# Optimization experiments

Hardware: AMD Instinct MI355X
Metric: run time of the kernel (lower is better)

The kernel has to match this reference:

```python
import jax, jax.numpy as jnp
import numpy as np

N_P, N_A, N_T = 20000, 10000, 5000
D_IN, D_OUT = 512, 256
E_P, E_A, E_T = 320000, 160000, 80000


def setup_inputs() -> dict:
    key = jax.random.key(0)
    ks = iter(jax.random.split(key, 64))

    def nrm(shape, scale=1.0):
        return jax.random.normal(next(ks), shape, dtype=jnp.float32) * scale

    def xav(shape):
        # xavier_uniform-like scale (gain 1.414), normal draw is fine for a baseline
        return nrm(shape, 1.414 * (2.0 / (shape[0] + shape[1])) ** 0.5)

    def edges(ne, n_src, n_dst):
        src = jax.random.randint(next(ks), (ne,), 0, n_src, dtype=jnp.int32)
        dst = jax.random.randint(next(ks), (ne,), 0, n_dst, dtype=jnp.int32)
        w = jax.random.uniform(next(ks), (ne,), dtype=jnp.float32) / 16.0  # ~normalized adj values
        return src, dst, w

    d = {}
    d["x_p"] = nrm((N_P, D_IN))
    d["x_a"] = nrm((N_A, D_IN))
    d["x_t"] = nrm((N_T, D_IN))
    d["e_p_a_src"], d["e_p_a_dst"], d["e_p_a_w"] = edges(E_P, N_A, N_P)
    d["e_p_t_src"], d["e_p_t_dst"], d["e_p_t_w"] = edges(E_P, N_T, N_P)
    d["e_a_p_src"], d["e_a_p_dst"], d["e_a_p_w"] = edges(E_A, N_P, N_A)
    d["e_a_t_src"], d["e_a_t_dst"], d["e_a_t_w"] = edges(E_A, N_T, N_A)
    d["e_t_p_src"], d["e_t_p_dst"], d["e_t_p_w"] = edges(E_T, N_P, N_T)
    d["e_t_a_src"], d["e_t_a_dst"], d["e_t_a_w"] = edges(E_T, N_A, N_T)
    # parameters for each target type k: W_proj per neighbor, w_self, w_share, w_att, w_cat, bias
    for k, nbs in (("p", ("a", "t")), ("a", ("p", "t")), ("t", ("p", "a"))):
        for nb in nbs:
            d[f"W_{k}_{nb}"] = xav((D_IN, D_OUT))
        d[f"ws_{k}"] = xav((D_IN, D_OUT))
        d[f"wsh_{k}"] = xav((D_OUT, D_OUT))
        d[f"watt_{k}"] = xav((2 * D_OUT, 1))
        d[f"wcat_{k}"] = xav((2 * D_OUT, D_OUT))
        d[f"b_{k}"] = xav((1, D_OUT))
    return d


def _hete_agg(x_self, w_self, w_share, w_att, w_cat, bias, nb_inputs):
    """nb_inputs: list of (x_nb, W_proj, src, dst, edge_w). Faithful to HeteAggregateLayer."""
    n = x_self.shape[0]
    self_ft = (x_self @ w_self) @ w_share  # [n, d]
    # per-relation: project -> spmm (gather + weighted segment-sum over dst) -> share
    nb_fts = [
        jax.ops.segment_sum((x_nb @ Wp)[src] * ew[:, None], dst, num_segments=n) @ w_share
        for (x_nb, Wp, src, dst, ew) in nb_inputs
    ]
    L = len(nb_fts)
    # e = leaky_relu(cat([cat(nb_ft,0), self_ft.repeat(L,1)],1) @ w_att)  -> [L*n, 1]
    e = jnp.concatenate(
        [jax.nn.leaky_relu(jnp.concatenate([f, self_ft], axis=1) @ w_att) for f in nb_fts],
        axis=0,
    )
    # NOTE: faithful replication of the original `e.view(-1, L)` reshape semantics
    att = jax.nn.softmax(e.reshape(n, L), axis=1)  # [n, L]
    agg = nb_fts[0] * att[:, 0:1]
    for i in range(1, L):
        agg = agg + nb_fts[i] * att[:, i : i + 1]
    return jnp.concatenate([agg, self_ft], axis=1) @ w_cat + bias


def reference(x_p, x_a, x_t,
              e_p_a_src, e_p_a_dst, e_p_a_w, e_p_t_src, e_p_t_dst, e_p_t_w,
              e_a_p_src, e_a_p_dst, e_a_p_w, e_a_t_src, e_a_t_dst, e_a_t_w,
              e_t_p_src, e_t_p_dst, e_t_p_w, e_t_a_src, e_t_a_dst, e_t_a_w,
              W_p_a, W_p_t, ws_p, wsh_p, watt_p, wcat_p, b_p,
              W_a_p, W_a_t, ws_a, wsh_a, watt_a, wcat_a, b_a,
              W_t_p, W_t_a, ws_t, wsh_t, watt_t, wcat_t, b_t):
    out_p = _hete_agg(x_p, ws_p, wsh_p, watt_p, wcat_p, b_p,
                      [(x_a, W_p_a, e_p_a_src, e_p_a_dst, e_p_a_w),
                       (x_t, W_p_t, e_p_t_src, e_p_t_dst, e_p_t_w)])
    out_a = _hete_agg(x_a, ws_a, wsh_a, watt_a, wcat_a, b_a,
                      [(x_p, W_a_p, e_a_p_src, e_a_p_dst, e_a_p_w),
                       (x_t, W_a_t, e_a_t_src, e_a_t_dst, e_a_t_w)])
    out_t = _hete_agg(x_t, ws_t, wsh_t, watt_t, wcat_t, b_t,
                      [(x_p, W_t_p, e_t_p_src, e_t_p_dst, e_t_p_w),
                       (x_a, W_t_a, e_t_a_src, e_t_a_dst, e_t_a_w)])
    return (out_p, out_a, out_t)
```

## Files before the change

kernel.cpp:

```cpp
#include <hip/hip_runtime.h>

namespace {

typedef short s16x8 __attribute__((ext_vector_type(8)));
typedef float f32x4 __attribute__((ext_vector_type(4)));

__device__ __forceinline__ float bf2f(unsigned short u) {
  return __uint_as_float(((unsigned)u) << 16);
}
__device__ __forceinline__ unsigned short f2bf(float f) {
  unsigned u = __float_as_uint(f);
  u += 0x7fffu + ((u >> 16) & 1u);
  return (unsigned short)(u >> 16);
}

typedef __attribute__((address_space(3))) unsigned int lds_u32;
typedef __attribute__((address_space(1))) const unsigned int glob_u32;
__device__ __forceinline__ void gl16(const void* g, void* l) {
  __builtin_amdgcn_global_load_lds((glob_u32*)g, (lds_u32*)l, 16, 0, 0);
}

__global__ __launch_bounds__(256) void cvt_x3(const float* __restrict__ x0,
                                              const float* __restrict__ x1,
                                              const float* __restrict__ x2,
                                              unsigned short* __restrict__ out) {
  size_t i = ((size_t)blockIdx.x * 256 + threadIdx.x) * 8;
  const float* src;
  size_t off;
  if (i < (size_t)20000 * 512) { src = x0; off = i; }
  else if (i < (size_t)30000 * 512) { src = x1; off = i - (size_t)20000 * 512; }
  else { src = x2; off = i - (size_t)30000 * 512; }
  float4 a = *(const float4*)(src + off);
  float4 b = *(const float4*)(src + off + 4);
  s16x8 v;
  v[0] = (short)f2bf(a.x); v[1] = (short)f2bf(a.y);
  v[2] = (short)f2bf(a.z); v[3] = (short)f2bf(a.w);
  v[4] = (short)f2bf(b.x); v[5] = (short)f2bf(b.y);
  v[6] = (short)f2bf(b.z); v[7] = (short)f2bf(b.w);
  *(s16x8*)(out + i) = v;
}

struct Tc6 { const float* src[6]; unsigned short* dst[6]; int R[6]; };
__global__ __launch_bounds__(256) void transpose_cvt(Tc6 a) {
  int mat = blockIdx.z;
  int R = a.R[mat];
  int r0 = blockIdx.y * 32, c0 = blockIdx.x * 32;
  if (r0 >= R) return;
  const float* __restrict__ src = a.src[mat];
  unsigned short* __restrict__ dst = a.dst[mat];
  __shared__ float T[32][33];
  int tx = threadIdx.x & 31, ty = threadIdx.x >> 5;
  #pragma unroll
  for (int j = 0; j < 4; ++j) {
    int r = ty + j * 8;
    T[r][tx] = src[(size_t)(r0 + r) * 256 + c0 + tx];
  }
  __syncthreads();
  #pragma unroll
  for (int j = 0; j < 4; ++j) {
    int c = ty + j * 8;
    dst[(size_t)(c0 + c) * R + r0 + tx] = f2bf(T[tx][c]);
  }
}

struct Comb9 { const unsigned short* A[9]; const float* B[9]; unsigned short* C[9]; };
__global__ __launch_bounds__(256) void combine_mfma(Comb9 g) {
  int z = blockIdx.z;
  const unsigned short* __restrict__ A = g.A[z];
  const float* __restrict__ B = g.B[z];
  unsigned short* __restrict__ C = g.C[z];
  int row0 = blockIdx.y * 128;
  int col0 = blockIdx.x * 128;
  __shared__ unsigned short As[128 * 40];
  __shared__ unsigned short Bs[128 * 40];
  int tid = threadIdx.x, lane = tid & 63, w = tid >> 6;
  int quad = lane >> 4, m16 = lane & 15;
  f32x4 acc[2][8];
  #pragma unroll
  for (int r = 0; r < 2; ++r)
    #pragma unroll
    for (int c = 0; c < 8; ++c) acc[r][c] = (f32x4){0.f, 0.f, 0.f, 0.f};
  for (int k0 = 0; k0 < 256; k0 += 32) {
    #pragma unroll
    for (int i = 0; i < 2; ++i) {
      int ch = tid + i * 256;
      int m = ch >> 2, kk = (ch & 3) * 8;
      *(s16x8*)&As[m * 40 + kk] = *(const s16x8*)(A + (size_t)(row0 + m) * 256 + k0 + kk);
      const float4* bp = (const float4*)(B + (size_t)(col0 + m) * 256 + k0 + kk);
      float4 b0 = bp[0], b1 = bp[1];
      s16x8 bv;
      bv[0] = (short)f2bf(b0.x); bv[1] = (short)f2bf(b0.y);
      bv[2] = (short)f2bf(b0.z); bv[3] = (short)f2bf(b0.w);
      bv[4] = (short)f2bf(b1.x); bv[5] = (short)f2bf(b1.y);
      bv[6] = (short)f2bf(b1.z); bv[7] = (short)f2bf(b1.w);
      *(s16x8*)&Bs[m * 40 + kk] = bv;
    }
    __syncthreads();
    s16x8 af[2], bf[8];
    #pragma unroll
    for (int r = 0; r < 2; ++r)
      af[r] = *(const s16x8*)&As[(w * 32 + r * 16 + m16) * 40 + quad * 8];
    #pragma unroll
    for (int c = 0; c < 8; ++c)
      bf[c] = *(const s16x8*)&Bs[(c * 16 + m16) * 40 + quad * 8];
    #pragma unroll
    for (int r = 0; r < 2; ++r)
      #pragma unroll
      for (int c = 0; c < 8; ++c)
        acc[r][c] = __builtin_amdgcn_mfma_f32_16x16x32_bf16(af[r], bf[c], acc[r][c], 0, 0, 0);
    __syncthreads();
  }
  #pragma unroll
  for (int r = 0; r < 2; ++r)
    #pragma unroll
    for (int i = 0; i < 4; ++i) {
      int row = row0 + w * 32 + r * 16 + quad * 4 + i;
      #pragma unroll
      for (int c = 0; c < 8; ++c)
        C[(size_t)row * 512 + col0 + c * 16 + m16] = f2bf(acc[r][c][i]);
    }
}

struct Proj9 { const unsigned short* A[9]; const unsigned short* Bt[9]; unsigned short* C[9]; int M[9]; };
__global__ __launch_bounds__(256) void proj_mfma9(Proj9 g) {
  int z = blockIdx.z;
  int M = g.M[z];
  int row0 = blockIdx.y * 128;
  if (row0 >= M) return;
  int col0 = blockIdx.x * 128;
  const unsigned short* __restrict__ A = g.A[z];
  const unsigned short* __restrict__ Bt = g.Bt[z];
  unsigned short* __restrict__ C = g.C[z];
  __shared__ unsigned short As[128 * 32];
  __shared__ unsigned short Bs[128 * 32];
  int tid = threadIdx.x, lane = tid & 63, w = tid >> 6;
  int quad = lane >> 4, m16 = lane & 15;
  int lr = lane >> 2, lk = (lane & 3) * 8;
  int r0g = row0 + w * 32 + lr;
  int r1g = r0g + 16;
  const unsigned short* a0p = A + (size_t)(r0g < M ? r0g : M - 1) * 512 + lk;
  const unsigned short* a1p = A + (size_t)(r1g < M ? r1g : M - 1) * 512 + lk;
  const unsigned short* b0p = Bt + (size_t)(col0 + w * 32 + lr) * 512 + lk;
  const unsigned short* b1p = b0p + (size_t)16 * 512;
  unsigned short* as0 = &As[w * 1024];
  unsigned short* as1 = &As[w * 1024 + 512];
  unsigned short* bs0 = &Bs[w * 1024];
  unsigned short* bs1 = &Bs[w * 1024 + 512];
  int wr = (w & 1) * 64, wc = (w >> 1) * 64;
  f32x4 acc[4][4];
  #pragma unroll
  for (int r = 0; r < 4; ++r)
    #pragma unroll
    for (int c = 0; c < 4; ++c) acc[r][c] = (f32x4){0.f, 0.f, 0.f, 0.f};
  for (int k0 = 0; k0 < 512; k0 += 32) {
    gl16(a0p + k0, as0);
    gl16(a1p + k0, as1);
    gl16(b0p + k0, bs0);
    gl16(b1p + k0, bs1);
    __syncthreads();
    s16x8 af[4], bf[4];
    #pragma unroll
    for (int r = 0; r < 4; ++r)
      af[r] = *(const s16x8*)&As[(wr + r * 16 + m16) * 32 + quad * 8];
    #pragma unroll
    for (int c = 0; c < 4; ++c)
      bf[c] = *(const s16x8*)&Bs[(wc + c * 16 + m16) * 32 + quad * 8];
    #pragma unroll
    for (int r = 0; r < 4; ++r)
      #pragma unroll
      for (int c = 0; c < 4; ++c)
        acc[r][c] = __builtin_amdgcn_mfma_f32_16x16x32_bf16(af[r], bf[c], acc[r][c], 0, 0, 0);
    __syncthreads();
  }
  #pragma unroll
  for (int r = 0; r < 4; ++r)
    #pragma unroll
    for (int i = 0; i < 4; ++i) {
      int row = row0 + wr + r * 16 + quad * 4 + i;
      if (row < M) {
        #pragma unroll
        for (int c = 0; c < 4; ++c)
          C[(size_t)row * 256 + col0 + wc + c * 16 + m16] = f2bf(acc[r][c][i]);
      }
    }
}

struct Edges6 { const int* src[6]; const int* dst[6]; const float* w[6]; int nE[6]; int cbase[6]; };

#define BSH 9
#define NB2 137
#define CAP2 10240
#define NOV 65536
#define CH 1024
#define NPAY 1120000

__global__ __launch_bounds__(256) void bin1(Edges6 ep, int* __restrict__ counts,
                                            int* __restrict__ bcur, int* __restrict__ ovcnt,
                                            unsigned long long* __restrict__ rec2,
                                            unsigned long long* __restrict__ ovbuf) {
  int rho = blockIdx.y;
  int nE = ep.nE[rho];
  int chunk = blockIdx.x * CH;
  if (chunk >= nE) return;
  int n = nE - chunk; if (n > CH) n = CH;
  const int* __restrict__ srcp = ep.src[rho];
  const int* __restrict__ dstp = ep.dst[rho];
  const float* __restrict__ wp = ep.w[rho];
  int cb = ep.cbase[rho];
  __shared__ int h[256], excl[256], lcur[256], gbase[256];
  __shared__ int wsum[4];
  __shared__ unsigned long long stage[CH];
  int t = threadIdx.x;
  h[t] = 0;
  gbase[t] = 0;
  __syncthreads();
  int gd[4]; unsigned pv[4];
  #pragma unroll
  for (int j = 0; j < 4; ++j) {
    int idx = t + j * 256;
    gd[j] = -1;
    if (idx < n) {
      int e = chunk + idx;
      int g = cb + dstp[e];
      if (g < 0) g = 0;
      if (g > 69999) g = 69999;
      gd[j] = g;
      pv[j] = (((unsigned)f2bf(wp[e])) << 16) | ((unsigned)srcp[e] & 0x7fffu);
      atomicAdd(&counts[g], 1);
      atomicAdd(&h[g >> BSH], 1);
    }
  }
  __syncthreads();
  int hv = h[t];
  int lane = t & 63, wv = t >> 6;
  int v = hv;
  #pragma unroll
  for (int off = 1; off < 64; off <<= 1) {
    int u = __shfl_up(v, off, 64);
    if (lane >= off) v += u;
  }
  if (lane == 63) wsum[wv] = v;
  __syncthreads();
  int add = 0;
  #pragma unroll
  for (int k = 0; k < 3; ++k)
    if (k < wv) add += wsum[k];
  v += add;
  int ex = v - hv;
  excl[t] = ex;
  lcur[t] = ex;
  if (t < NB2 && hv > 0) gbase[t] = atomicAdd(&bcur[t], hv);
  __syncthreads();
  #pragma unroll
  for (int j = 0; j < 4; ++j) {
    if (gd[j] >= 0) {
      int b = gd[j] >> BSH;
      int slot = atomicAdd(&lcur[b], 1);
      if (slot >= 0 && slot < CH)
        stage[slot] = ((unsigned long long)(unsigned)gd[j] << 32) | pv[j];
    }
  }
  __syncthreads();
  for (int s = t; s < n; s += 256) {
    int lo = 0, hi = NB2 - 1;
    while (lo < hi) {
      int mid = (lo + hi + 1) >> 1;
      if (excl[mid] <= s) lo = mid; else hi = mid - 1;
    }
    int b = lo;
    int gp = gbase[b] + (s - excl[b]);
    if (gp >= 0 && gp < CAP2) rec2[(size_t)b * CAP2 + gp] = stage[s];
    else { int op = atomicAdd(ovcnt, 1); ovbuf[op & (NOV - 1)] = stage[s]; }
  }
}

__global__ __launch_bounds__(256) void scan1(const int* __restrict__ cnt, int* __restrict__ out,
                                             int* __restrict__ part, int len) {
  __shared__ int sh[256];
  int base = blockIdx.x * 2048 + threadIdx.x * 8;
  int v[8];
  int s = 0;
  #pragma unroll
  for (int j = 0; j < 8; ++j) {
    int i = base + j;
    int x = (i < len) ? cnt[i] : 0;
    v[j] = s;
    s += x;
  }
  sh[threadIdx.x] = s;
  __syncthreads();
  for (int off = 1; off < 256; off <<= 1) {
    int t = (threadIdx.x >= off) ? sh[threadIdx.x - off] : 0;
    __syncthreads();
    sh[threadIdx.x] += t;
    __syncthreads();
  }
  int texcl = sh[threadIdx.x] - s;
  #pragma unroll
  for (int j = 0; j < 8; ++j) {
    int i = base + j;
    if (i < len) out[i] = texcl + v[j];
  }
  if (threadIdx.x == 255) part[blockIdx.x] = sh[255];
}

__global__ void scan2(int* __restrict__ part, int nb, int* __restrict__ total_out) {
  __shared__ int sh[64];
  int t = threadIdx.x;
  int v = (t < nb) ? part[t] : 0;
  sh[t] = v;
  __syncthreads();
  for (int off = 1; off < 64; off <<= 1) {
    int x = (t >= off) ? sh[t - off] : 0;
    __syncthreads();
    sh[t] += x;
    __syncthreads();
  }
  if (t < nb) part[t] = sh[t] - v;
  if (t == 63) *total_out = sh[63];
}

__global__ __launch_bounds__(256) void scan3(int* __restrict__ offs,
                                             const int* __restrict__ part, int len) {
  int i = blockIdx.x * 256 + threadIdx.x;
  if (i >= len) return;
  offs[i] += part[i >> 11];
}

__global__ __launch_bounds__(512) void fine2(const int* __restrict__ offs,
                                             const int* __restrict__ bcur,
                                             const unsigned long long* __restrict__ rec2,
                                             const int* __restrict__ ovcnt,
                                             const unsigned long long* __restrict__ ovbuf,
                                             unsigned int* __restrict__ pay) {
  int b = blockIdx.x;
  __shared__ int cur[512];
  int t = threadIdx.x;
  {
    int gd = (b << BSH) + t;
    cur[t] = (gd < 70000) ? offs[gd] : 0;
  }
  __syncthreads();
  int nrec = bcur[b];
  nrec = nrec < CAP2 ? nrec : CAP2;
  const unsigned long long* rp = rec2 + (size_t)b * CAP2;
  for (int i = t; i < nrec; i += 512) {
    unsigned long long r = rp[i];
    int ld = (int)(r >> 32) & 511;
    int pos = atomicAdd(&cur[ld], 1);
    if (pos >= 0 && pos < NPAY) pay[pos] = (unsigned)r;
  }
  int ovn = *ovcnt;
  ovn = ovn < NOV ? ovn : NOV;
  for (int i = t; i < ovn; i += 512) {
    unsigned long long r = ovbuf[i];
    int gd = (int)(r >> 32);
    if ((gd >> BSH) == b) {
      int pos = atomicAdd(&cur[gd & 511], 1);
      if (pos >= 0 && pos < NPAY) pay[pos] = (unsigned)r;
    }
  }
}

struct Gather6 { const unsigned short* proj[6]; unsigned short* out[6]; int cb[6]; int n[6]; };
__global__ __launch_bounds__(256) void gather_all(Gather6 g, const int* __restrict__ offs,
                                                  const unsigned int* __restrict__ pay) {
  int rho = blockIdx.y;
  int n = g.n[rho];
  int d = blockIdx.x * 4 + (threadIdx.x >> 6);
  if (d >= n) return;
  int lane = threadIdx.x & 63, half = lane >> 5, l32 = lane & 31;
  const unsigned short* __restrict__ proj = g.proj[rho];
  const int* of = offs + g.cb[rho];
  int s0 = of[d], s1 = of[d + 1];
  float acc[8] = {};
  int e = s0 + half;
  for (; e + 2 < s1; e += 4) {
    unsigned int u0 = pay[e], u1 = pay[e + 2];
    float wt0 = bf2f((unsigned short)(u0 >> 16));
    float wt1 = bf2f((unsigned short)(u1 >> 16));
    s16x8 v0 = *(const s16x8*)(proj + (size_t)(u0 & 0xffffu) * 256 + l32 * 8);
    s16x8 v1 = *(const s16x8*)(proj + (size_t)(u1 & 0xffffu) * 256 + l32 * 8);
    #pragma unroll
    for (int j = 0; j < 8; ++j) {
      acc[j] = fmaf(bf2f((unsigned short)v0[j]), wt0, acc[j]);
      acc[j] = fmaf(bf2f((unsigned short)v1[j]), wt1, acc[j]);
    }
  }
  if (e < s1) {
    unsigned int u = pay[e];
    float wt = bf2f((unsigned short)(u >> 16));
    s16x8 v = *(const s16x8*)(proj + (size_t)(u & 0xffffu) * 256 + l32 * 8);
    #pragma unroll
    for (int j = 0; j < 8; ++j) acc[j] = fmaf(bf2f((unsigned short)v[j]), wt, acc[j]);
  }
  #pragma unroll
  for (int j = 0; j < 8; ++j) acc[j] += __shfl(acc[j], lane ^ 32, 64);
  if (half == 0) {
    s16x8 o;
    #pragma unroll
    for (int j = 0; j < 8; ++j) o[j] = (short)f2bf(acc[j]);
    *(s16x8*)(g.out[rho] + (size_t)d * 256 + l32 * 8) = o;
  }
}

struct Att3 { const unsigned short* nb[3]; const unsigned short* self[3];
              const float* watt[3]; float* att[3]; int n[3]; };
__global__ __launch_bounds__(256) void e_att3(Att3 g) {
  int z = blockIdx.z;
  int n = g.n[z];
  int wv = threadIdx.x >> 6;
  int idx = blockIdx.x * 4 + wv;
  int lane = threadIdx.x & 63;
  __shared__ float ev[4];
  float sum = 0.f;
  if (idx < 2 * n) {
    int i = idx < n ? idx : idx - n;
    ushort4 v  = *(const ushort4*)(g.nb[z] + (size_t)idx * 256 + (lane << 2));
    ushort4 sv = *(const ushort4*)(g.self[z] + (size_t)i * 256 + (lane << 2));
    float4 wa = *(const float4*)(g.watt[z] + (lane << 2));
    float4 wb = *(const float4*)(g.watt[z] + 256 + (lane << 2));
    sum = bf2f(v.x) * wa.x + bf2f(v.y) * wa.y + bf2f(v.z) * wa.z + bf2f(v.w) * wa.w +
          bf2f(sv.x) * wb.x + bf2f(sv.y) * wb.y + bf2f(sv.z) * wb.z + bf2f(sv.w) * wb.w;
    #pragma unroll
    for (int off = 32; off > 0; off >>= 1) sum += __shfl_down(sum, off, 64);
  }
  if (lane == 0) ev[wv] = sum;
  __syncthreads();
  if (threadIdx.x < 2) {
    int base = blockIdx.x * 4 + threadIdx.x * 2;
    if (base < 2 * n) {
      float f0 = ev[threadIdx.x * 2], f1 = ev[threadIdx.x * 2 + 1];
      f0 = f0 > 0.f ? f0 : 0.01f * f0;
      f1 = f1 > 0.f ? f1 : 0.01f * f1;
      float m = fmaxf(f0, f1);
      float a = expf(f0 - m), b = expf(f1 - m);
      float inv = 1.f / (a + b);
      g.att[z][base] = a * inv;
      g.att[z][base + 1] = b * inv;
    }
  }
}

struct Fin3 { const unsigned short* nb[3]; const unsigned short* self[3]; const float* att[3];
              const unsigned short* Wt[3]; const float* bias[3]; float* out[3]; int M[3]; };
__global__ __launch_bounds__(256, 3) void final_mfma3(Fin3 g) {
  int z = blockIdx.z;
  int M = g.M[z];
  int row0 = blockIdx.y * 64;
  if (row0 >= M) return;
  const unsigned short* __restrict__ nbft = g.nb[z];
  const unsigned short* __restrict__ selfb = g.self[z];
  const float* __restrict__ att = g.att[z];
  const unsigned short* __restrict__ Wt = g.Wt[z];
  __shared__ unsigned short As[64 * 40];
  __shared__ unsigned short Bs[256 * 40];
  int tid = threadIdx.x, lane = tid & 63, w = tid >> 6;
  int quad = lane >> 4, m16 = lane & 15;
  int am = tid >> 2, akk = (tid & 3) * 8;
  int gr = row0 + am;
  float a0 = 0.f, a1 = 0.f;
  if (gr < M) { a0 = att[2 * gr]; a1 = att[2 * gr + 1]; }
  f32x4 acc[4][4];
  #pragma unroll
  for (int r = 0; r < 4; ++r)
    #pragma unroll
    for (int c = 0; c < 4; ++c) acc[r][c] = (f32x4){0.f, 0.f, 0.f, 0.f};

  s16x8 pu0 = {}, pu1 = {};
  s16x8 pb[4];

  auto loadA = [&](int k0) {
    int kg = k0 + akk;
    if (gr < M) {
      if (kg < 256) {
        pu0 = *(const s16x8*)(nbft + (size_t)gr * 256 + kg);
        pu1 = *(const s16x8*)(nbft + ((size_t)M + gr) * 256 + kg);
      } else {
        pu0 = *(const s16x8*)(selfb + (size_t)gr * 256 + (kg - 256));
      }
    }
  };
  auto loadB = [&](int k0) {
    #pragma unroll
    for (int i = 0; i < 4; ++i) {
      int ch = tid + i * 256;
      int m = ch >> 2, kk = (ch & 3) * 8;
      pb[i] = *(const s16x8*)(Wt + (size_t)m * 512 + k0 + kk);
    }
  };
  auto storeLDS = [&](int k0) {
    int kg = k0 + akk;
    s16x8 v = {};
    if (gr < M) {
      if (kg < 256) {
        #pragma unroll
        for (int j = 0; j < 8; ++j)
          v[j] = (short)f2bf(fmaf(a0, bf2f((unsigned short)pu0[j]),
                                  a1 * bf2f((unsigned short)pu1[j])));
      } else {
        v = pu0;
      }
    }
    *(s16x8*)&As[am * 40 + akk] = v;
    #pragma unroll
    for (int i = 0; i < 4; ++i) {
      int ch = tid + i * 256;
      int m = ch >> 2, kk = (ch & 3) * 8;
      *(s16x8*)&Bs[m * 40 + kk] = pb[i];
    }
  };

  loadA(0); loadB(0); storeLDS(0);
  __syncthreads();
  for (int k0 = 0; k0 < 512; k0 += 32) {
    int kn = k0 + 32;
    if (kn < 512) { loadA(kn); loadB(kn); }
    s16x8 af[4], bf[4];
    #pragma unroll
    for (int r = 0; r < 4; ++r)
      af[r] = *(const s16x8*)&As[(r * 16 + m16) * 40 + quad * 8];
    #pragma unroll
    for (int c = 0; c < 4; ++c)
      bf[c] = *(const s16x8*)&Bs[(w * 64 + c * 16 + m16) * 40 + quad * 8];
    #pragma unroll
    for (int r = 0; r < 4; ++r)
      #pragma unroll
      for (int c = 0; c < 4; ++c)
        acc[r][c] = __builtin_amdgcn_mfma_f32_16x16x32_bf16(af[r], bf[c], acc[r][c], 0, 0, 0);
    __syncthreads();
    if (kn < 512) {
      storeLDS(kn);
      __syncthreads();
    }
  }
  const float* __restrict__ bias = g.bias[z];
  float* __restrict__ out = g.out[z];
  #pragma unroll
  for (int r = 0; r < 4; ++r)
    #pragma unroll
    for (int i = 0; i < 4; ++i) {
      int row = row0 + r * 16 + quad * 4 + i;
      if (row < M) {
        #pragma unroll
        for (int c = 0; c < 4; ++c) {
          int col = w * 64 + c * 16 + m16;
          out[(size_t)row * 256 + col] = acc[r][c][i] + bias[col];
        }
      }
    }
}

}

extern "C" void kernel_launch(void* const* d_in, const int* in_sizes, int n_in,
                              void* d_out, int out_size, void* d_ws, size_t ws_size,
                              hipStream_t stream) {
  (void)in_sizes; (void)n_in; (void)out_size; (void)ws_size;
  const float* x[3] = {(const float*)d_in[0], (const float*)d_in[1], (const float*)d_in[2]};

  char* p = (char*)d_ws;
  unsigned short* projfull = (unsigned short*)p;  p += (size_t)105000 * 256 * 2;
  unsigned short* nbft = (unsigned short*)p;      p += (size_t)70000 * 256 * 2;
  unsigned short* wcatbt = (unsigned short*)p;    p += (size_t)3 * 256 * 512 * 2;
  int* offs = (int*)p;                            p += (size_t)70004 * 4;
  int* counts = (int*)p;                          p += (size_t)70000 * 4;
  int* bcur = (int*)p;                            p += 160 * 4;
  int* ovcnt = (int*)p;                           p += 16;
  int* part = (int*)p;                            p += 256;
  float* att_buf = (float*)p;                     p += (size_t)70000 * 4;
  unsigned int* csr_pay = (unsigned int*)p;       p += (size_t)1120000 * 4;
  unsigned short* wshT = nbft;
  unsigned short* Wcbt = (unsigned short*)((char*)nbft + 393216);
  unsigned long long* rec2 = (unsigned long long*)projfull;
  unsigned long long* ovbuf = rec2 + (size_t)NB2 * CAP2;
  unsigned short* xb = (unsigned short*)d_out;

  const int n_of[3] = {20000, 10000, 5000};
  const int nbt[3][2] = {{1, 2}, {0, 2}, {0, 1}};
  const int ebase[3][2] = {{3, 6}, {9, 12}, {15, 18}};
  const int nE3[3] = {320000, 160000, 80000};
  const size_t out_off[3] = {0, (size_t)20000 * 256, (size_t)30000 * 256};
  const int tstart[3] = {0, 15000, 40000};
  const int selfoff[3] = {70000, 90000, 100000};
  const int nboff[3] = {0, 40000, 60000};
  const int xboff[3] = {0, 20000, 30000};

  cvt_x3<<<dim3(8750), 256, 0, stream>>>(x[0], x[1], x[2], xb);

  Tc6 tc;
  for (int t = 0; t < 3; ++t) {
    tc.src[t] = (const float*)d_in[21 + t * 7 + 3];
    tc.dst[t] = wshT + (size_t)t * 256 * 256;
    tc.R[t] = 256;
    tc.src[3 + t] = (const float*)d_in[21 + t * 7 + 5];
    tc.dst[3 + t] = wcatbt + (size_t)t * 256 * 512;
    tc.R[3 + t] = 512;
  }
  transpose_cvt<<<dim3(8, 16, 6), 256, 0, stream>>>(tc);

  Comb9 c9;
  for (int t = 0; t < 3; ++t) {
    int wb = 21 + t * 7;
    for (int j = 0; j < 3; ++j) {
      int combo = t * 3 + j;
      c9.A[combo] = wshT + (size_t)t * 256 * 256;
      c9.B[combo] = (const float*)d_in[wb + j];
      c9.C[combo] = Wcbt + (size_t)combo * 256 * 512;
    }
  }
  combine_mfma<<<dim3(4, 2, 9), 256, 0, stream>>>(c9);

  Edges6 ep;
  const int cbase[6] = {0, 20000, 40000, 50000, 60000, 65000};
  for (int t = 0; t < 3; ++t)
    for (int r = 0; r < 2; ++r) {
      int rho = t * 2 + r, eb = ebase[t][r];
      ep.src[rho] = (const int*)d_in[eb];
      ep.dst[rho] = (const int*)d_in[eb + 1];
      ep.w[rho] = (const float*)d_in[eb + 2];
      ep.nE[rho] = nE3[t];
      ep.cbase[rho] = cbase[rho];
    }
  hipMemsetAsync(counts, 0, (size_t)70000 * 4 + 160 * 4 + 16, stream);
  bin1<<<dim3(313, 6), 256, 0, stream>>>(ep, counts, bcur, ovcnt, rec2, ovbuf);
  scan1<<<35, 256, 0, stream>>>(counts, offs, part, 70000);
  scan2<<<1, 64, 0, stream>>>(part, 35, offs + 70000);
  scan3<<<274, 256, 0, stream>>>(offs, part, 70000);
  fine2<<<NB2, 512, 0, stream>>>(offs, bcur, rec2, ovcnt, ovbuf, csr_pay);

  Proj9 pj;
  for (int t = 0; t < 3; ++t) {
    int nb0 = nbt[t][0], nb1 = nbt[t][1];
    int m0 = n_of[nb0];
    pj.A[t * 3 + 0] = xb + (size_t)xboff[nb0] * 512;
    pj.C[t * 3 + 0] = projfull + (size_t)tstart[t] * 256;
    pj.M[t * 3 + 0] = m0;
    pj.A[t * 3 + 1] = xb + (size_t)xboff[nb1] * 512;
    pj.C[t * 3 + 1] = projfull + (size_t)(tstart[t] + m0) * 256;
    pj.M[t * 3 + 1] = n_of[nb1];
    pj.A[t * 3 + 2] = xb + (size_t)xboff[t] * 512;
    pj.C[t * 3 + 2] = projfull + (size_t)selfoff[t] * 256;
    pj.M[t * 3 + 2] = n_of[t];
    for (int j = 0; j < 3; ++j)
      pj.Bt[t * 3 + j] = Wcbt + (size_t)(t * 3 + j) * 256 * 512;
  }
  proj_mfma9<<<dim3(2, 157, 9), 256, 0, stream>>>(pj);

  Gather6 gt;
  for (int t = 0; t < 3; ++t) {
    int m0 = n_of[nbt[t][0]];
    for (int r = 0; r < 2; ++r) {
      int rho = t * 2 + r;
      gt.proj[rho] = projfull + (size_t)(tstart[t] + (r ? m0 : 0)) * 256;
      gt.out[rho] = nbft + (size_t)(nboff[t] + r * n_of[t]) * 256;
      gt.cb[rho] = cbase[rho];
      gt.n[rho] = n_of[t];
    }
  }
  gather_all<<<dim3(5000, 6), 256, 0, stream>>>(gt, offs, csr_pay);

  Att3 at;
  for (int t = 0; t < 3; ++t) {
    at.nb[t] = nbft + (size_t)nboff[t] * 256;
    at.self[t] = projfull + (size_t)selfoff[t] * 256;
    at.watt[t] = (const float*)d_in[21 + t * 7 + 4];
    at.att[t] = att_buf + nboff[t];
    at.n[t] = n_of[t];
  }
  e_att3<<<dim3(10000, 1, 3), 256, 0, stream>>>(at);

  Fin3 fn;
  for (int t = 0; t < 3; ++t) {
    fn.nb[t] = nbft + (size_t)nboff[t] * 256;
    fn.self[t] = projfull + (size_t)selfoff[t] * 256;
    fn.att[t] = att_buf + nboff[t];
    fn.Wt[t] = wcatbt + (size_t)t * 256 * 512;
    fn.bias[t] = (const float*)d_in[21 + t * 7 + 6];
    fn.out[t] = (float*)d_out + out_off[t];
    fn.M[t] = n_of[t];
  }
  final_mfma3<<<dim3(1, 313, 3), 256, 0, stream>>>(fn);
}
```

Measured before the change: 433.3 us.

## Replace global per-destination count atomics with per-bucket LDS histogram pass

Drops the global atomicAdd on per-destination counts inside bin1 and adds a cnt2 kernel that rebuilds the counts from the bucketed records using LDS atomics, one block per bucket. Bucket reservations are rounded up to multiples of 8, with sentinel padding records that fine2 and cnt2 skip, and bucket capacity is raised. This is meant to cut contended global atomics on the 70k counters, at the cost of an extra kernel launch and a second read of all the records.

```diff
diff --git a/kernel.cpp b/kernel.cpp
--- a/kernel.cpp
+++ b/kernel.cpp
@@ -189,12 +189,12 @@
 
 #define BSH 9
 #define NB2 137
-#define CAP2 10240
+#define CAP2 16384
 #define NOV 65536
 #define CH 1024
 #define NPAY 1120000
 
-__global__ __launch_bounds__(256) void bin1(Edges6 ep, int* __restrict__ counts,
+__global__ __launch_bounds__(256) void bin1(Edges6 ep,
                                             int* __restrict__ bcur, int* __restrict__ ovcnt,
                                             unsigned long long* __restrict__ rec2,
                                             unsigned long long* __restrict__ ovbuf) {
@@ -207,7 +207,7 @@
   const int* __restrict__ dstp = ep.dst[rho];
   const float* __restrict__ wp = ep.w[rho];
   int cb = ep.cbase[rho];
-  __shared__ int h[256], excl[256], lcur[256], gbase[256];
+  __shared__ int h[256], excl[256], lcur[256], gbase[256], rsv[256];
   __shared__ int wsum[4];
   __shared__ unsigned long long stage[CH];
   int t = threadIdx.x;
@@ -226,7 +226,6 @@
       if (g > 69999) g = 69999;
       gd[j] = g;
       pv[j] = (((unsigned)f2bf(wp[e])) << 16) | ((unsigned)srcp[e] & 0x7fffu);
-      atomicAdd(&counts[g], 1);
       atomicAdd(&h[g >> BSH], 1);
     }
   }
@@ -249,7 +248,12 @@
   int ex = v - hv;
   excl[t] = ex;
   lcur[t] = ex;
-  if (t < NB2 && hv > 0) gbase[t] = atomicAdd(&bcur[t], hv);
+  int rv = 0;
+  if (t < NB2 && hv > 0) {
+    rv = (hv + 7) & ~7;
+    gbase[t] = atomicAdd(&bcur[t], rv);
+  }
+  rsv[t] = rv;
   __syncthreads();
   #pragma unroll
   for (int j = 0; j < 4; ++j) {
@@ -272,6 +276,43 @@
     if (gp >= 0 && gp < CAP2) rec2[(size_t)b * CAP2 + gp] = stage[s];
     else { int op = atomicAdd(ovcnt, 1); ovbuf[op & (NOV - 1)] = stage[s]; }
   }
+  for (int b = t; b < NB2; b += 256) {
+    int hvb = h[b], rvb = rsv[b], gb = gbase[b];
+    for (int k = hvb; k < rvb; ++k) {
+      int gp = gb + k;
+      if (gp >= 0 && gp < CAP2) rec2[(size_t)b * CAP2 + gp] = 0xFFFFFFFFFFFFFFFFull;
+    }
+  }
+}
+
+__global__ __launch_bounds__(256) void cnt2(const int* __restrict__ bcur,
+                                            const unsigned long long* __restrict__ rec2,
+                                            const int* __restrict__ ovcnt,
+                                            const unsigned long long* __restrict__ ovbuf,
+                                            int* __restrict__ counts) {
+  int b = blockIdx.x;
+  __shared__ int c[512];
+  int t = threadIdx.x;
+  c[t] = 0; c[t + 256] = 0;
+  __syncthreads();
+  int nrec = bcur[b];
+  nrec = nrec < CAP2 ? nrec : CAP2;
+  const unsigned long long* rp = rec2 + (size_t)b * CAP2;
+  for (int i = t; i < nrec; i += 256) {
+    int gd = (int)(rp[i] >> 32);
+    if (gd >= 0) atomicAdd(&c[gd & 511], 1);
+  }
+  int ovn = *ovcnt;
+  ovn = ovn < NOV ? ovn : NOV;
+  for (int i = t; i < ovn; i += 256) {
+    int gd = (int)(ovbuf[i] >> 32);
+    if (gd >= 0 && (gd >> BSH) == b) atomicAdd(&c[gd & 511], 1);
+  }
+  __syncthreads();
+  int g0 = (b << BSH) + t;
+  if (g0 < 70000) counts[g0] = c[t];
+  int g1 = g0 + 256;
+  if (g1 < 70000) counts[g1] = c[t + 256];
 }
 
 __global__ __launch_bounds__(256) void scan1(const int* __restrict__ cnt, int* __restrict__ out,
@@ -346,8 +387,9 @@
   const unsigned long long* rp = rec2 + (size_t)b * CAP2;
   for (int i = t; i < nrec; i += 512) {
     unsigned long long r = rp[i];
-    int ld = (int)(r >> 32) & 511;
-    int pos = atomicAdd(&cur[ld], 1);
+    int gd = (int)(r >> 32);
+    if (gd < 0) continue;
+    int pos = atomicAdd(&cur[gd & 511], 1);
     if (pos >= 0 && pos < NPAY) pay[pos] = (unsigned)r;
   }
   int ovn = *ovcnt;
@@ -355,7 +397,7 @@
   for (int i = t; i < ovn; i += 512) {
     unsigned long long r = ovbuf[i];
     int gd = (int)(r >> 32);
-    if ((gd >> BSH) == b) {
+    if (gd >= 0 && (gd >> BSH) == b) {
       int pos = atomicAdd(&cur[gd & 511], 1);
       if (pos >= 0 && pos < NPAY) pay[pos] = (unsigned)r;
     }
@@ -622,8 +664,9 @@
       ep.nE[rho] = nE3[t];
       ep.cbase[rho] = cbase[rho];
     }
-  hipMemsetAsync(counts, 0, (size_t)70000 * 4 + 160 * 4 + 16, stream);
-  bin1<<<dim3(313, 6), 256, 0, stream>>>(ep, counts, bcur, ovcnt, rec2, ovbuf);
+  hipMemsetAsync(bcur, 0, 160 * 4 + 16, stream);
+  bin1<<<dim3(313, 6), 256, 0, stream>>>(ep, bcur, ovcnt, rec2, ovbuf);
+  cnt2<<<NB2, 256, 0, stream>>>(bcur, rec2, ovcnt, ovbuf, counts);
   scan1<<<35, 256, 0, stream>>>(counts, offs, part, 70000);
   scan2<<<1, 64, 0, stream>>>(part, 35, offs + 70000);
   scan3<<<274, 256, 0, stream>>>(offs, part, 70000);
```

Measured after the change: 406.4 us. 1.07x faster.
